# Optimization experiments

Measured on AMD Instinct MI355X. Metric: run time of the kernel, lower is better.

The kernel has to match this reference:

```python
import jax, jax.numpy as jnp
import numpy as np

F, V, D, B = 3, 512, 8192, 64


def setup_inputs() -> dict:
    key = jax.random.key(0)
    k1, k2 = jax.random.split(key)
    # bipolar (MAP) codebooks: (f, v, d) in {-1, +1}
    codebooks = jnp.sign(jax.random.normal(k1, (F, V, D), dtype=jnp.float32))
    codebooks = jnp.where(codebooks == 0, 1.0, codebooks)
    # ground-truth factors -> inputs = bind (elementwise product) of one codevector per factor
    idx = jax.random.randint(k2, (B, F), 0, V)
    picked = codebooks[jnp.arange(F)[None, :], idx]          # (b, f, d)
    inputs = jnp.prod(picked, axis=1)                         # (b, d)
    # init estimates: bundle (superposition) of each codebook, signed, broadcast to batch
    init = jnp.sign(jnp.sum(codebooks, axis=1))               # (f, d)
    init = jnp.where(init == 0, 1.0, init)
    init_estimates = jnp.broadcast_to(init, (B, F, D)).astype(jnp.float32)
    return {"inputs": inputs, "init_estimates": init_estimates,
            "codebooks": codebooks, "iterations": 10}


def reference(inputs, init_estimates, codebooks, iterations):
    f = init_estimates.shape[-2]

    def step(est):
        # MAP inverse is identity; inv_others[:, j] = prod_{i != j} est[:, i]
        rolled = jnp.stack([jnp.roll(est, i, axis=-2) for i in range(1, f)], axis=-2)  # (b,f,f-1,d)
        inv_others = jnp.prod(rolled, axis=-2)                 # (b, f, d)  multibind
        new_est = inputs[:, None, :] * inv_others              # bind       (b, f, d)
        sim = jnp.einsum('bfd,fvd->bfv', new_est, codebooks)   # codebook similarity
        return jnp.sign(jnp.einsum('bfv,fvd->bfd', sim, codebooks))

    def cond(c):
        est, old, cnt, done = c
        return (cnt < iterations) & jnp.logical_not(done)

    def body(c):
        est, old, cnt, done = c
        new = step(est)
        done = jnp.all(new == old)
        return (new, new, cnt + 1, done)

    carry0 = (init_estimates, init_estimates, jnp.int32(0), jnp.array(False))
    est, _, cnt, _ = jax.lax.while_loop(cond, body, carry0)

    # cleanup: nearest codevector per factor (argmax dot similarity)
    sims = jnp.einsum('bfd,fvd->bfv', est, codebooks)
    outcome = jnp.argmax(sims, axis=-1)                        # (b, f) int indices
    return outcome, cnt - 1
```

## Files before the change

kernel.cpp:

```cpp
#include <hip/hip_runtime.h>

#define F 3
#define V 512
#define D 8192
#define B 64
#define ITERS 10
#define DW 256

typedef __bf16 bf16_t;
typedef __bf16 bf16x8 __attribute__((ext_vector_type(8)));
typedef float f32x4 __attribute__((ext_vector_type(4)));
typedef unsigned int u32;
typedef unsigned long long u64;


__global__ __launch_bounds__(256) void k_init_tr(const float* __restrict__ Csrc,
                                                 bf16_t* __restrict__ CbT,
                                                 u32* __restrict__ Cbits) {
  int f = blockIdx.z, vt = blockIdx.y, dt = blockIdx.x;
  __shared__ bf16_t tile[64 * 65];
  int t = threadIdx.x;
  int lane = t & 63;
  int v0 = vt * 64, d0 = dt * 64;
#pragma unroll
  for (int p = 0; p < 16; ++p) {
    int q = t + 256 * p;
    int i = q >> 6, j = q & 63;
    float x = Csrc[((long)(f * V + v0 + i)) * D + d0 + j];
    tile[i * 65 + j] = (bf16_t)x;
    u64 bal = __ballot(x < 0.f);
    if (lane == 0) {
      int v = v0 + i;
      uint2 wp;
      wp.x = (u32)(bal & 0xffffffffull);
      wp.y = (u32)(bal >> 32);
      *(uint2*)&Cbits[(((f * 64 + (dt >> 1)) * 512) + v) * 4 + (dt & 1) * 2] = wp;
    }
  }
  __syncthreads();
#pragma unroll
  for (int p = 0; p < 16; ++p) {
    int q = t + 256 * p;
    int jj = q >> 6, ii = q & 63;
    CbT[((long)f * D + d0 + jj) * V + v0 + ii] = tile[ii * 65 + jj];
  }
}

__global__ void k_init_pack(const float* __restrict__ inputs, const float* __restrict__ ie,
                            u32* __restrict__ in_bits, u32* __restrict__ es0,
                            u32* __restrict__ ez0, int* __restrict__ flags) {
  int tid = blockIdx.x * blockDim.x + threadIdx.x;
  int lane = tid & 63;
  int gw = tid >> 6;
  int NW = (gridDim.x * blockDim.x) >> 6;
  const int IN_W = B * (D / 64);
  const int EST_W = B * F * (D / 64);
  for (int c = gw; c < IN_W + EST_W; c += NW) {
    if (c < IN_W) {
      int b = c >> 7, dc = c & 127;
      float x = inputs[(long)b * D + dc * 64 + lane];
      u64 bal = __ballot(x < 0.f);
      if (lane == 0) {
        in_bits[b * DW + dc * 2] = (u32)(bal & 0xffffffffull);
        in_bits[b * DW + dc * 2 + 1] = (u32)(bal >> 32);
      }
    } else {
      int cc = c - IN_W;
      int bf = cc >> 7, dc = cc & 127;
      float x = ie[(long)bf * D + dc * 64 + lane];
      u64 bs = __ballot(x < 0.f);
      u64 bz = __ballot(x == 0.f);
      if (lane == 0) {
        es0[bf * DW + dc * 2] = (u32)(bs & 0xffffffffull);
        es0[bf * DW + dc * 2 + 1] = (u32)(bs >> 32);
        ez0[bf * DW + dc * 2] = (u32)(bz & 0xffffffffull);
        ez0[bf * DW + dc * 2 + 1] = (u32)(bz >> 32);
      }
    }
  }
  if (tid < 32) flags[tid] = 0;
}

__global__ __launch_bounds__(256) void k_sim(const u32* __restrict__ Cbits,
                                             const u32* __restrict__ in_bits,
                                             const u32* __restrict__ es0,
                                             const u32* __restrict__ ez0,
                                             const u32* __restrict__ es1,
                                             const u32* __restrict__ ez1,
                                             int* __restrict__ simBase,
                                             const int* __restrict__ anydiff,
                                             const int* __restrict__ hzp, int iter) {
  const int t = threadIdx.x, lane = t & 63;
  const int gw = blockIdx.x * 4 + (t >> 6);
  const int vg = gw & 7, bp = (gw >> 3) & 31, f = gw >> 8;
  const int b0 = bp * 2;
  const bool is_final = (iter >= ITERS);
  const u32 *es, *ez;
  int* sim;
  if (is_final) {
    int first0 = ITERS;
    for (int i = 0; i < ITERS; ++i)
      if (anydiff[i] == 0) { first0 = i; break; }
    int par = (first0 < ITERS) ? ((first0 + 1) & 1) : 0;
    es = par ? es1 : es0;
    ez = par ? ez1 : ez0;
    sim = simBase + ITERS * (F * B * V);
  } else {
    for (int i = 0; i < iter; ++i)
      if (anydiff[i] == 0) return;
    es = (iter & 1) ? es1 : es0;
    ez = (iter & 1) ? ez1 : ez0;
    sim = simBase + iter * (F * B * V);
  }
  const int hz = *hzp;

  u32 As0[4], As1[4], Az0[4], Az1[4];
  if (is_final) {
    const int i0 = (b0 * F + f) * DW, i1 = ((b0 + 1) * F + f) * DW;
#pragma unroll
    for (int r = 0; r < 4; ++r) {
      int o = r * 64 + lane;
      As0[r] = es[i0 + o];
      As1[r] = es[i1 + o];
    }
    if (hz) {
#pragma unroll
      for (int r = 0; r < 4; ++r) {
        int o = r * 64 + lane;
        Az0[r] = ~ez[i0 + o];
        Az1[r] = ~ez[i1 + o];
      }
    }
  } else {
    const int f1 = (f + 1) % 3, f2 = (f + 2) % 3;
    const int a0 = (b0 * F + f1) * DW, a1 = (b0 * F + f2) * DW;
    const int c0 = ((b0 + 1) * F + f1) * DW, c1 = ((b0 + 1) * F + f2) * DW;
    const int n0 = b0 * DW, n1 = (b0 + 1) * DW;
#pragma unroll
    for (int r = 0; r < 4; ++r) {
      int o = r * 64 + lane;
      As0[r] = in_bits[n0 + o] ^ es[a0 + o] ^ es[a1 + o];
      As1[r] = in_bits[n1 + o] ^ es[c0 + o] ^ es[c1 + o];
    }
    if (hz) {
#pragma unroll
      for (int r = 0; r < 4; ++r) {
        int o = r * 64 + lane;
        Az0[r] = ~(ez[a0 + o] | ez[a1 + o]);
        Az1[r] = ~(ez[c0 + o] | ez[c1 + o]);
      }
    }
  }

  int nzc0 = D, nzc1 = D;
  if (hz) {
    int p0 = 0, p1 = 0;
#pragma unroll
    for (int r = 0; r < 4; ++r) {
      p0 += __popc(Az0[r]);
      p1 += __popc(Az1[r]);
    }
    for (int off = 32; off; off >>= 1) {
      p0 += __shfl_xor(p0, off, 64);
      p1 += __shfl_xor(p1, off, 64);
    }
    nzc0 = p0;
    nzc1 = p1;
  }

  int acc0 = 0, acc1 = 0;
  const uint4* Cp = (const uint4*)Cbits + ((long)f * 64) * 512 + vg * 64 + lane;
  if (!hz) {
#pragma unroll
    for (int r = 0; r < 4; ++r) {
#pragma unroll
      for (int i = 0; i < 16; ++i) {
        uint4 c = Cp[(r * 16 + i) * 512];
        const int k = i * 4;
        u32 a;
        a = (u32)__builtin_amdgcn_readlane((int)As0[r], k + 0); acc0 += __popc(c.x ^ a);
        a = (u32)__builtin_amdgcn_readlane((int)As0[r], k + 1); acc0 += __popc(c.y ^ a);
        a = (u32)__builtin_amdgcn_readlane((int)As0[r], k + 2); acc0 += __popc(c.z ^ a);
        a = (u32)__builtin_amdgcn_readlane((int)As0[r], k + 3); acc0 += __popc(c.w ^ a);
        a = (u32)__builtin_amdgcn_readlane((int)As1[r], k + 0); acc1 += __popc(c.x ^ a);
        a = (u32)__builtin_amdgcn_readlane((int)As1[r], k + 1); acc1 += __popc(c.y ^ a);
        a = (u32)__builtin_amdgcn_readlane((int)As1[r], k + 2); acc1 += __popc(c.z ^ a);
        a = (u32)__builtin_amdgcn_readlane((int)As1[r], k + 3); acc1 += __popc(c.w ^ a);
      }
    }
  } else {
#pragma unroll
    for (int r = 0; r < 4; ++r) {
#pragma unroll
      for (int i = 0; i < 16; ++i) {
        uint4 c = Cp[(r * 16 + i) * 512];
        const int k = i * 4;
        u32 a, z;
        a = (u32)__builtin_amdgcn_readlane((int)As0[r], k + 0);
        z = (u32)__builtin_amdgcn_readlane((int)Az0[r], k + 0); acc0 += __popc((c.x ^ a) & z);
        a = (u32)__builtin_amdgcn_readlane((int)As0[r], k + 1);
        z = (u32)__builtin_amdgcn_readlane((int)Az0[r], k + 1); acc0 += __popc((c.y ^ a) & z);
        a = (u32)__builtin_amdgcn_readlane((int)As0[r], k + 2);
        z = (u32)__builtin_amdgcn_readlane((int)Az0[r], k + 2); acc0 += __popc((c.z ^ a) & z);
        a = (u32)__builtin_amdgcn_readlane((int)As0[r], k + 3);
        z = (u32)__builtin_amdgcn_readlane((int)Az0[r], k + 3); acc0 += __popc((c.w ^ a) & z);
        a = (u32)__builtin_amdgcn_readlane((int)As1[r], k + 0);
        z = (u32)__builtin_amdgcn_readlane((int)Az1[r], k + 0); acc1 += __popc((c.x ^ a) & z);
        a = (u32)__builtin_amdgcn_readlane((int)As1[r], k + 1);
        z = (u32)__builtin_amdgcn_readlane((int)Az1[r], k + 1); acc1 += __popc((c.y ^ a) & z);
        a = (u32)__builtin_amdgcn_readlane((int)As1[r], k + 2);
        z = (u32)__builtin_amdgcn_readlane((int)Az1[r], k + 2); acc1 += __popc((c.z ^ a) & z);
        a = (u32)__builtin_amdgcn_readlane((int)As1[r], k + 3);
        z = (u32)__builtin_amdgcn_readlane((int)Az1[r], k + 3); acc1 += __popc((c.w ^ a) & z);
      }
    }
  }
  const int v = vg * 64 + lane;
  sim[(f * B + b0) * V + v] = nzc0 - 2 * acc0;
  sim[(f * B + b0 + 1) * V + v] = nzc1 - 2 * acc1;
}

__global__ __launch_bounds__(256) void k_upd(const int* __restrict__ simBase,
                                             const bf16_t* __restrict__ CbT,
                                             u32* __restrict__ es0, u32* __restrict__ ez0,
                                             u32* __restrict__ es1, u32* __restrict__ ez1,
                                             int* __restrict__ anydiff,
                                             int* __restrict__ hzp, int iter) {
  const int f = blockIdx.y;
  const int d0 = blockIdx.x * 128;
  for (int i = 0; i < iter; ++i)
    if (anydiff[i] == 0) return;
  const u32* esIn = (iter & 1) ? es1 : es0;
  const u32* ezIn = (iter & 1) ? ez1 : ez0;
  u32* esOut = (iter & 1) ? es0 : es1;
  u32* ezOut = (iter & 1) ? ez0 : ez1;
  const int* sim = simBase + iter * (F * B * V) + f * (B * V);

  __shared__ __attribute__((aligned(16))) bf16_t lAh[64 * 88];
  __shared__ __attribute__((aligned(16))) bf16_t lAl[64 * 88];
  __shared__ __attribute__((aligned(16))) bf16_t lB[128 * 88];

  const int t = threadIdx.x;
  const int lane = t & 63, w = t >> 6;
  const int lm = lane & 15, quad = lane >> 4;

  f32x4 zero = {0.f, 0.f, 0.f, 0.f};
  f32x4 accH[4][2], accL[4][2];
#pragma unroll
  for (int mt = 0; mt < 4; ++mt)
#pragma unroll
    for (int nt = 0; nt < 2; ++nt) { accH[mt][nt] = zero; accL[mt][nt] = zero; }

  for (int c = 0; c < 8; ++c) {
    const int vb = c * 64;
    __syncthreads();
#pragma unroll
    for (int p = 0; p < 2; ++p) {
      int q = t + 256 * p;
      int b = q >> 3, vv = (q & 7) * 8;
      const int* sp = sim + b * V + vb + vv;
#pragma unroll
      for (int i = 0; i < 8; ++i) {
        int si = sp[i];
        lAh[b * 88 + vv + i] = (bf16_t)(float)(si >> 8);
        lAl[b * 88 + vv + i] = (bf16_t)(float)(si & 255);
      }
    }
#pragma unroll
    for (int p = 0; p < 4; ++p) {
      int q = t + 256 * p;
      int r = q >> 3, vv = (q & 7) * 8;
      *(bf16x8*)&lB[r * 88 + vv] =
          *(const bf16x8*)(CbT + ((long)f * D + d0 + r) * V + vb + vv);
    }
    __syncthreads();
#pragma unroll
    for (int ks2 = 0; ks2 < 2; ++ks2) {
      const int kb = ks2 * 32 + quad * 8;
      bf16x8 bf0 = *(const bf16x8*)&lB[(w * 32 + lm) * 88 + kb];
      bf16x8 bf1 = *(const bf16x8*)&lB[(w * 32 + 16 + lm) * 88 + kb];
#pragma unroll
      for (int mt = 0; mt < 4; ++mt) {
        bf16x8 ah = *(const bf16x8*)&lAh[(mt * 16 + lm) * 88 + kb];
        bf16x8 al = *(const bf16x8*)&lAl[(mt * 16 + lm) * 88 + kb];
        accH[mt][0] = __builtin_amdgcn_mfma_f32_16x16x32_bf16(ah, bf0, accH[mt][0], 0, 0, 0);
        accH[mt][1] = __builtin_amdgcn_mfma_f32_16x16x32_bf16(ah, bf1, accH[mt][1], 0, 0, 0);
        accL[mt][0] = __builtin_amdgcn_mfma_f32_16x16x32_bf16(al, bf0, accL[mt][0], 0, 0, 0);
        accL[mt][1] = __builtin_amdgcn_mfma_f32_16x16x32_bf16(al, bf1, accL[mt][1], 0, 0, 0);
      }
    }
  }
  const int W = blockIdx.x * 4 + w;
  bool anyd = false, zf = false;
#pragma unroll
  for (int mt = 0; mt < 4; ++mt)
#pragma unroll
    for (int r = 0; r < 4; ++r) {
      float v0 = 256.f * accH[mt][0][r] + accL[mt][0][r];
      float v1 = 256.f * accH[mt][1][r] + accL[mt][1][r];
      u64 s0 = __ballot(v0 < 0.f);
      u64 s1 = __ballot(v1 < 0.f);
      u64 z0 = __ballot(v0 == 0.f);
      u64 z1 = __ballot(v1 == 0.f);
      zf |= ((z0 | z1) != 0ull);
      if (lm == 0) {
        u32 ws = (u32)((s0 >> (quad * 16)) & 0xffffull) |
                 (((u32)((s1 >> (quad * 16)) & 0xffffull)) << 16);
        u32 wz = (u32)((z0 >> (quad * 16)) & 0xffffull) |
                 (((u32)((z1 >> (quad * 16)) & 0xffffull)) << 16);
        int b = mt * 16 + quad * 4 + r;
        int idx = (b * F + f) * DW + W;
        esOut[idx] = ws;
        ezOut[idx] = wz;
        anyd |= (esIn[idx] != ws) || (ezIn[idx] != wz);
      }
    }
  if (__any(anyd) && lane == 0) atomicOr(&anydiff[iter], 1);
  if (zf && lane == 0) atomicOr(hzp, 1);
}

__global__ __launch_bounds__(64) void k_out(const int* __restrict__ simBase,
                                            const int* __restrict__ anydiff,
                                            int* __restrict__ out) {
  const int* sim = simBase + ITERS * (F * B * V);
  int bid = blockIdx.x;
  int b = bid / F, f = bid % F;
  int lane = threadIdx.x;
  const int* row = sim + (f * B + b) * V;
  int best = -2147483647;
  int bidx = 0;
#pragma unroll
  for (int i = 0; i < V / 64; ++i) {
    int v = lane + 64 * i;
    int x = row[v];
    if (x > best) { best = x; bidx = v; }
  }
  for (int off = 32; off; off >>= 1) {
    int ov = __shfl_down(best, off, 64);
    int oi = __shfl_down(bidx, off, 64);
    if (ov > best || (ov == best && oi < bidx)) { best = ov; bidx = oi; }
  }
  if (lane == 0) out[b * F + f] = bidx;
  if (bid == 0 && lane == 0) {
    int first0 = ITERS;
    for (int i = 0; i < ITERS; ++i) {
      if (anydiff[i] == 0) { first0 = i; break; }
    }
    int cnt = (first0 < ITERS) ? (first0 + 1) : ITERS;
    out[B * F] = cnt - 1;
  }
}

extern "C" void kernel_launch(void* const* d_in, const int* in_sizes, int n_in,
                              void* d_out, int out_size, void* d_ws, size_t ws_size,
                              hipStream_t stream) {
  const float* inputs    = (const float*)d_in[0];
  const float* init_est  = (const float*)d_in[1];
  const float* codebooks = (const float*)d_in[2];

  char* w = (char*)d_ws;
  size_t o = 0;
  auto alloc = [&](size_t bytes) -> void* {
    void* p = w + o;
    o = (o + bytes + 255) & ~(size_t)255;
    return p;
  };
  bf16_t* CbT  = (bf16_t*)alloc((size_t)F * D * V * 2);
  u32* Cbits   = (u32*)alloc((size_t)F * 64 * 512 * 4 * 4);
  u32* in_bits = (u32*)alloc((size_t)B * DW * 4);
  u32* es0     = (u32*)alloc((size_t)B * F * DW * 4);
  u32* ez0     = (u32*)alloc((size_t)B * F * DW * 4);
  u32* es1     = (u32*)alloc((size_t)B * F * DW * 4);
  u32* ez1     = (u32*)alloc((size_t)B * F * DW * 4);
  int* simBase = (int*)alloc((size_t)(ITERS + 1) * F * B * V * 4);
  int* flags   = (int*)alloc(128);
  int* anydiff = flags;
  int* hz      = flags + 16;

  k_init_tr<<<dim3(128, 8, 3), 256, 0, stream>>>(codebooks, CbT, Cbits);
  k_init_pack<<<1024, 256, 0, stream>>>(inputs, init_est, in_bits, es0, ez0, flags);

  for (int j = 0; j < ITERS; ++j) {
    k_sim<<<192, 256, 0, stream>>>(Cbits, in_bits, es0, ez0, es1, ez1, simBase, anydiff, hz, j);
    k_upd<<<dim3(64, 3), 256, 0, stream>>>(simBase, CbT, es0, ez0, es1, ez1, anydiff, hz, j);
  }
  k_sim<<<192, 256, 0, stream>>>(Cbits, in_bits, es0, ez0, es1, ez1, simBase, anydiff, hz, ITERS);
  k_out<<<B * F, 64, 0, stream>>>(simBase, anydiff, (int*)d_out);
}
```

Baseline: 498.6 us.

## Fuse iteration loop into one persistent kernel with software grid barriers

Replaces the 21 per-iteration sim/update launches plus the output kernel with one persistent kernel of 192 blocks. Blocks synchronise through an atomic counter/generation grid barrier, and the loop exits early on convergence instead of launching no-op kernels. This removes kernel launch gaps and shrinks the sim buffer to a single reused slot. Correctness now relies on all 192 blocks being co-resident, which a plain launch does not guarantee. Flag initialisation moves into k_init_tr, and the hz flag is now set from the initial estimates.

```diff
diff --git a/kernel.cpp b/kernel.cpp
--- a/kernel.cpp
+++ b/kernel.cpp
@@ -6,6 +6,7 @@
 #define B 64
 #define ITERS 10
 #define DW 256
+#define NBLK 192
 
 typedef __bf16 bf16_t;
 typedef __bf16 bf16x8 __attribute__((ext_vector_type(8)));
@@ -16,12 +17,14 @@
 
 __global__ __launch_bounds__(256) void k_init_tr(const float* __restrict__ Csrc,
                                                  bf16_t* __restrict__ CbT,
-                                                 u32* __restrict__ Cbits) {
+                                                 u32* __restrict__ Cbits,
+                                                 int* __restrict__ flags) {
   int f = blockIdx.z, vt = blockIdx.y, dt = blockIdx.x;
   __shared__ bf16_t tile[64 * 65];
   int t = threadIdx.x;
   int lane = t & 63;
   int v0 = vt * 64, d0 = dt * 64;
+  if (f == 0 && vt == 0 && dt == 0 && t < 32) flags[t] = 0;
 #pragma unroll
   for (int p = 0; p < 16; ++p) {
     int q = t + 256 * p;
@@ -75,278 +78,287 @@
         es0[bf * DW + dc * 2 + 1] = (u32)(bs >> 32);
         ez0[bf * DW + dc * 2] = (u32)(bz & 0xffffffffull);
         ez0[bf * DW + dc * 2 + 1] = (u32)(bz >> 32);
-      }
-    }
-  }
-  if (tid < 32) flags[tid] = 0;
-}
-
-__global__ __launch_bounds__(256) void k_sim(const u32* __restrict__ Cbits,
-                                             const u32* __restrict__ in_bits,
-                                             const u32* __restrict__ es0,
-                                             const u32* __restrict__ ez0,
-                                             const u32* __restrict__ es1,
-                                             const u32* __restrict__ ez1,
-                                             int* __restrict__ simBase,
-                                             const int* __restrict__ anydiff,
-                                             const int* __restrict__ hzp, int iter) {
-  const int t = threadIdx.x, lane = t & 63;
-  const int gw = blockIdx.x * 4 + (t >> 6);
-  const int vg = gw & 7, bp = (gw >> 3) & 31, f = gw >> 8;
-  const int b0 = bp * 2;
-  const bool is_final = (iter >= ITERS);
-  const u32 *es, *ez;
-  int* sim;
-  if (is_final) {
-    int first0 = ITERS;
-    for (int i = 0; i < ITERS; ++i)
-      if (anydiff[i] == 0) { first0 = i; break; }
-    int par = (first0 < ITERS) ? ((first0 + 1) & 1) : 0;
-    es = par ? es1 : es0;
-    ez = par ? ez1 : ez0;
-    sim = simBase + ITERS * (F * B * V);
-  } else {
-    for (int i = 0; i < iter; ++i)
-      if (anydiff[i] == 0) return;
-    es = (iter & 1) ? es1 : es0;
-    ez = (iter & 1) ? ez1 : ez0;
-    sim = simBase + iter * (F * B * V);
-  }
-  const int hz = *hzp;
-
-  u32 As0[4], As1[4], Az0[4], Az1[4];
-  if (is_final) {
-    const int i0 = (b0 * F + f) * DW, i1 = ((b0 + 1) * F + f) * DW;
-#pragma unroll
-    for (int r = 0; r < 4; ++r) {
-      int o = r * 64 + lane;
-      As0[r] = es[i0 + o];
-      As1[r] = es[i1 + o];
-    }
-    if (hz) {
-#pragma unroll
-      for (int r = 0; r < 4; ++r) {
-        int o = r * 64 + lane;
-        Az0[r] = ~ez[i0 + o];
-        Az1[r] = ~ez[i1 + o];
-      }
-    }
-  } else {
-    const int f1 = (f + 1) % 3, f2 = (f + 2) % 3;
-    const int a0 = (b0 * F + f1) * DW, a1 = (b0 * F + f2) * DW;
-    const int c0 = ((b0 + 1) * F + f1) * DW, c1 = ((b0 + 1) * F + f2) * DW;
-    const int n0 = b0 * DW, n1 = (b0 + 1) * DW;
-#pragma unroll
-    for (int r = 0; r < 4; ++r) {
-      int o = r * 64 + lane;
-      As0[r] = in_bits[n0 + o] ^ es[a0 + o] ^ es[a1 + o];
-      As1[r] = in_bits[n1 + o] ^ es[c0 + o] ^ es[c1 + o];
-    }
-    if (hz) {
-#pragma unroll
-      for (int r = 0; r < 4; ++r) {
-        int o = r * 64 + lane;
-        Az0[r] = ~(ez[a0 + o] | ez[a1 + o]);
-        Az1[r] = ~(ez[c0 + o] | ez[c1 + o]);
-      }
-    }
-  }
-
-  int nzc0 = D, nzc1 = D;
-  if (hz) {
-    int p0 = 0, p1 = 0;
-#pragma unroll
-    for (int r = 0; r < 4; ++r) {
-      p0 += __popc(Az0[r]);
-      p1 += __popc(Az1[r]);
-    }
-    for (int off = 32; off; off >>= 1) {
-      p0 += __shfl_xor(p0, off, 64);
-      p1 += __shfl_xor(p1, off, 64);
-    }
-    nzc0 = p0;
-    nzc1 = p1;
-  }
-
-  int acc0 = 0, acc1 = 0;
-  const uint4* Cp = (const uint4*)Cbits + ((long)f * 64) * 512 + vg * 64 + lane;
-  if (!hz) {
-#pragma unroll
-    for (int r = 0; r < 4; ++r) {
-#pragma unroll
-      for (int i = 0; i < 16; ++i) {
-        uint4 c = Cp[(r * 16 + i) * 512];
-        const int k = i * 4;
-        u32 a;
-        a = (u32)__builtin_amdgcn_readlane((int)As0[r], k + 0); acc0 += __popc(c.x ^ a);
-        a = (u32)__builtin_amdgcn_readlane((int)As0[r], k + 1); acc0 += __popc(c.y ^ a);
-        a = (u32)__builtin_amdgcn_readlane((int)As0[r], k + 2); acc0 += __popc(c.z ^ a);
-        a = (u32)__builtin_amdgcn_readlane((int)As0[r], k + 3); acc0 += __popc(c.w ^ a);
-        a = (u32)__builtin_amdgcn_readlane((int)As1[r], k + 0); acc1 += __popc(c.x ^ a);
-        a = (u32)__builtin_amdgcn_readlane((int)As1[r], k + 1); acc1 += __popc(c.y ^ a);
-        a = (u32)__builtin_amdgcn_readlane((int)As1[r], k + 2); acc1 += __popc(c.z ^ a);
-        a = (u32)__builtin_amdgcn_readlane((int)As1[r], k + 3); acc1 += __popc(c.w ^ a);
-      }
-    }
-  } else {
-#pragma unroll
-    for (int r = 0; r < 4; ++r) {
-#pragma unroll
-      for (int i = 0; i < 16; ++i) {
-        uint4 c = Cp[(r * 16 + i) * 512];
-        const int k = i * 4;
-        u32 a, z;
-        a = (u32)__builtin_amdgcn_readlane((int)As0[r], k + 0);
-        z = (u32)__builtin_amdgcn_readlane((int)Az0[r], k + 0); acc0 += __popc((c.x ^ a) & z);
-        a = (u32)__builtin_amdgcn_readlane((int)As0[r], k + 1);
-        z = (u32)__builtin_amdgcn_readlane((int)Az0[r], k + 1); acc0 += __popc((c.y ^ a) & z);
-        a = (u32)__builtin_amdgcn_readlane((int)As0[r], k + 2);
-        z = (u32)__builtin_amdgcn_readlane((int)Az0[r], k + 2); acc0 += __popc((c.z ^ a) & z);
-        a = (u32)__builtin_amdgcn_readlane((int)As0[r], k + 3);
-        z = (u32)__builtin_amdgcn_readlane((int)Az0[r], k + 3); acc0 += __popc((c.w ^ a) & z);
-        a = (u32)__builtin_amdgcn_readlane((int)As1[r], k + 0);
-        z = (u32)__builtin_amdgcn_readlane((int)Az1[r], k + 0); acc1 += __popc((c.x ^ a) & z);
-        a = (u32)__builtin_amdgcn_readlane((int)As1[r], k + 1);
-        z = (u32)__builtin_amdgcn_readlane((int)Az1[r], k + 1); acc1 += __popc((c.y ^ a) & z);
-        a = (u32)__builtin_amdgcn_readlane((int)As1[r], k + 2);
-        z = (u32)__builtin_amdgcn_readlane((int)Az1[r], k + 2); acc1 += __popc((c.z ^ a) & z);
-        a = (u32)__builtin_amdgcn_readlane((int)As1[r], k + 3);
-        z = (u32)__builtin_amdgcn_readlane((int)Az1[r], k + 3); acc1 += __popc((c.w ^ a) & z);
-      }
-    }
-  }
-  const int v = vg * 64 + lane;
-  sim[(f * B + b0) * V + v] = nzc0 - 2 * acc0;
-  sim[(f * B + b0 + 1) * V + v] = nzc1 - 2 * acc1;
-}
-
-__global__ __launch_bounds__(256) void k_upd(const int* __restrict__ simBase,
-                                             const bf16_t* __restrict__ CbT,
-                                             u32* __restrict__ es0, u32* __restrict__ ez0,
-                                             u32* __restrict__ es1, u32* __restrict__ ez1,
-                                             int* __restrict__ anydiff,
-                                             int* __restrict__ hzp, int iter) {
-  const int f = blockIdx.y;
-  const int d0 = blockIdx.x * 128;
-  for (int i = 0; i < iter; ++i)
-    if (anydiff[i] == 0) return;
-  const u32* esIn = (iter & 1) ? es1 : es0;
-  const u32* ezIn = (iter & 1) ? ez1 : ez0;
-  u32* esOut = (iter & 1) ? es0 : es1;
-  u32* ezOut = (iter & 1) ? ez0 : ez1;
-  const int* sim = simBase + iter * (F * B * V) + f * (B * V);
-
+        if (bz) atomicOr(&flags[16], 1);
+      }
+    }
+  }
+}
+
+__device__ inline void grid_sync(int* counter, int* gen) {
+  __syncthreads();
+  if (threadIdx.x == 0) {
+    __threadfence();
+    int g = __hip_atomic_load(gen, __ATOMIC_RELAXED, __HIP_MEMORY_SCOPE_AGENT);
+    int a = __hip_atomic_fetch_add(counter, 1, __ATOMIC_ACQ_REL, __HIP_MEMORY_SCOPE_AGENT);
+    if (a == NBLK - 1) {
+      __hip_atomic_store(counter, 0, __ATOMIC_RELAXED, __HIP_MEMORY_SCOPE_AGENT);
+      __hip_atomic_store(gen, g + 1, __ATOMIC_RELEASE, __HIP_MEMORY_SCOPE_AGENT);
+    } else {
+      while (__hip_atomic_load(gen, __ATOMIC_ACQUIRE, __HIP_MEMORY_SCOPE_AGENT) == g)
+        __builtin_amdgcn_s_sleep(2);
+    }
+    __threadfence();
+  }
+  __syncthreads();
+}
+
+__global__ __launch_bounds__(256) void k_fused(
+    const u32* __restrict__ Cbits, const u32* __restrict__ in_bits,
+    u32* __restrict__ es0, u32* __restrict__ ez0,
+    u32* __restrict__ es1, u32* __restrict__ ez1,
+    const bf16_t* __restrict__ CbT, int* __restrict__ sim,
+    int* __restrict__ flags, int* __restrict__ out) {
   __shared__ __attribute__((aligned(16))) bf16_t lAh[64 * 88];
   __shared__ __attribute__((aligned(16))) bf16_t lAl[64 * 88];
   __shared__ __attribute__((aligned(16))) bf16_t lB[128 * 88];
-
-  const int t = threadIdx.x;
-  const int lane = t & 63, w = t >> 6;
+  __shared__ int sh_hz, sh_conv;
+
+  int* bar_cnt = flags + 24;
+  int* bar_gen = flags + 25;
+
+  const int bid = blockIdx.x;
+  const int t = threadIdx.x, lane = t & 63, w = t >> 6;
   const int lm = lane & 15, quad = lane >> 4;
-
-  f32x4 zero = {0.f, 0.f, 0.f, 0.f};
-  f32x4 accH[4][2], accL[4][2];
-#pragma unroll
-  for (int mt = 0; mt < 4; ++mt)
-#pragma unroll
-    for (int nt = 0; nt < 2; ++nt) { accH[mt][nt] = zero; accL[mt][nt] = zero; }
-
-  for (int c = 0; c < 8; ++c) {
-    const int vb = c * 64;
+  const int gw = bid * 4 + w;
+  const int vg = gw & 7, bp = (gw >> 3) & 31, fs = gw >> 8;
+  const int b0 = bp * 2;
+  const int du = (bid & 63) * 128, fu = bid >> 6;
+
+  int parity = 0;
+  int done_iter = ITERS;
+
+  if (t == 0)
+    sh_hz = __hip_atomic_load(&flags[16], __ATOMIC_ACQUIRE, __HIP_MEMORY_SCOPE_AGENT);
+  __syncthreads();
+
+  auto sim_phase = [&](bool is_final, int hz) {
+    const u32* es = parity ? es1 : es0;
+    const u32* ez = parity ? ez1 : ez0;
+    u32 As0[4], As1[4], Az0[4], Az1[4];
+    if (is_final) {
+      const int i0 = (b0 * F + fs) * DW, i1 = ((b0 + 1) * F + fs) * DW;
+#pragma unroll
+      for (int r = 0; r < 4; ++r) {
+        int o = r * 64 + lane;
+        As0[r] = es[i0 + o];
+        As1[r] = es[i1 + o];
+      }
+      if (hz) {
+#pragma unroll
+        for (int r = 0; r < 4; ++r) {
+          int o = r * 64 + lane;
+          Az0[r] = ~ez[i0 + o];
+          Az1[r] = ~ez[i1 + o];
+        }
+      }
+    } else {
+      const int f1 = (fs + 1) % 3, f2 = (fs + 2) % 3;
+      const int a0 = (b0 * F + f1) * DW, a1 = (b0 * F + f2) * DW;
+      const int c0 = ((b0 + 1) * F + f1) * DW, c1 = ((b0 + 1) * F + f2) * DW;
+      const int n0 = b0 * DW, n1 = (b0 + 1) * DW;
+#pragma unroll
+      for (int r = 0; r < 4; ++r) {
+        int o = r * 64 + lane;
+        As0[r] = in_bits[n0 + o] ^ es[a0 + o] ^ es[a1 + o];
+        As1[r] = in_bits[n1 + o] ^ es[c0 + o] ^ es[c1 + o];
+      }
+      if (hz) {
+#pragma unroll
+        for (int r = 0; r < 4; ++r) {
+          int o = r * 64 + lane;
+          Az0[r] = ~(ez[a0 + o] | ez[a1 + o]);
+          Az1[r] = ~(ez[c0 + o] | ez[c1 + o]);
+        }
+      }
+    }
+
+    int nzc0 = D, nzc1 = D;
+    if (hz) {
+      int p0 = 0, p1 = 0;
+#pragma unroll
+      for (int r = 0; r < 4; ++r) {
+        p0 += __popc(Az0[r]);
+        p1 += __popc(Az1[r]);
+      }
+      for (int off = 32; off; off >>= 1) {
+        p0 += __shfl_xor(p0, off, 64);
+        p1 += __shfl_xor(p1, off, 64);
+      }
+      nzc0 = p0;
+      nzc1 = p1;
+    }
+
+    int acc0 = 0, acc1 = 0;
+    const uint4* Cp = (const uint4*)Cbits + ((long)fs * 64) * 512 + vg * 64 + lane;
+    if (!hz) {
+#pragma unroll
+      for (int r = 0; r < 4; ++r) {
+#pragma unroll
+        for (int i = 0; i < 16; ++i) {
+          uint4 c = Cp[(r * 16 + i) * 512];
+          const int k = i * 4;
+          u32 a;
+          a = (u32)__builtin_amdgcn_readlane((int)As0[r], k + 0); acc0 += __popc(c.x ^ a);
+          a = (u32)__builtin_amdgcn_readlane((int)As0[r], k + 1); acc0 += __popc(c.y ^ a);
+          a = (u32)__builtin_amdgcn_readlane((int)As0[r], k + 2); acc0 += __popc(c.z ^ a);
+          a = (u32)__builtin_amdgcn_readlane((int)As0[r], k + 3); acc0 += __popc(c.w ^ a);
+          a = (u32)__builtin_amdgcn_readlane((int)As1[r], k + 0); acc1 += __popc(c.x ^ a);
+          a = (u32)__builtin_amdgcn_readlane((int)As1[r], k + 1); acc1 += __popc(c.y ^ a);
+          a = (u32)__builtin_amdgcn_readlane((int)As1[r], k + 2); acc1 += __popc(c.z ^ a);
+          a = (u32)__builtin_amdgcn_readlane((int)As1[r], k + 3); acc1 += __popc(c.w ^ a);
+        }
+      }
+    } else {
+#pragma unroll
+      for (int r = 0; r < 4; ++r) {
+#pragma unroll
+        for (int i = 0; i < 16; ++i) {
+          uint4 c = Cp[(r * 16 + i) * 512];
+          const int k = i * 4;
+          u32 a, z;
+          a = (u32)__builtin_amdgcn_readlane((int)As0[r], k + 0);
+          z = (u32)__builtin_amdgcn_readlane((int)Az0[r], k + 0); acc0 += __popc((c.x ^ a) & z);
+          a = (u32)__builtin_amdgcn_readlane((int)As0[r], k + 1);
+          z = (u32)__builtin_amdgcn_readlane((int)Az0[r], k + 1); acc0 += __popc((c.y ^ a) & z);
+          a = (u32)__builtin_amdgcn_readlane((int)As0[r], k + 2);
+          z = (u32)__builtin_amdgcn_readlane((int)Az0[r], k + 2); acc0 += __popc((c.z ^ a) & z);
+          a = (u32)__builtin_amdgcn_readlane((int)As0[r], k + 3);
+          z = (u32)__builtin_amdgcn_readlane((int)Az0[r], k + 3); acc0 += __popc((c.w ^ a) & z);
+          a = (u32)__builtin_amdgcn_readlane((int)As1[r], k + 0);
+          z = (u32)__builtin_amdgcn_readlane((int)Az1[r], k + 0); acc1 += __popc((c.x ^ a) & z);
+          a = (u32)__builtin_amdgcn_readlane((int)As1[r], k + 1);
+          z = (u32)__builtin_amdgcn_readlane((int)Az1[r], k + 1); acc1 += __popc((c.y ^ a) & z);
+          a = (u32)__builtin_amdgcn_readlane((int)As1[r], k + 2);
+          z = (u32)__builtin_amdgcn_readlane((int)Az1[r], k + 2); acc1 += __popc((c.z ^ a) & z);
+          a = (u32)__builtin_amdgcn_readlane((int)As1[r], k + 3);
+          z = (u32)__builtin_amdgcn_readlane((int)Az1[r], k + 3); acc1 += __popc((c.w ^ a) & z);
+        }
+      }
+    }
+    const int v = vg * 64 + lane;
+    sim[(fs * B + b0) * V + v] = nzc0 - 2 * acc0;
+    sim[(fs * B + b0 + 1) * V + v] = nzc1 - 2 * acc1;
+  };
+
+  auto upd_phase = [&](int j) {
+    const u32* esIn = parity ? es1 : es0;
+    const u32* ezIn = parity ? ez1 : ez0;
+    u32* esOut = parity ? es0 : es1;
+    u32* ezOut = parity ? ez0 : ez1;
+    const int* simf = sim + fu * (B * V);
+
+    f32x4 zero = {0.f, 0.f, 0.f, 0.f};
+    f32x4 accH[4][2], accL[4][2];
+#pragma unroll
+    for (int mt = 0; mt < 4; ++mt)
+#pragma unroll
+      for (int nt = 0; nt < 2; ++nt) { accH[mt][nt] = zero; accL[mt][nt] = zero; }
+
+    for (int c = 0; c < 8; ++c) {
+      const int vb = c * 64;
+      __syncthreads();
+#pragma unroll
+      for (int p = 0; p < 2; ++p) {
+        int q = t + 256 * p;
+        int b = q >> 3, vv = (q & 7) * 8;
+        const int* sp = simf + b * V + vb + vv;
+#pragma unroll
+        for (int i = 0; i < 8; ++i) {
+          int si = sp[i];
+          lAh[b * 88 + vv + i] = (bf16_t)(float)(si >> 8);
+          lAl[b * 88 + vv + i] = (bf16_t)(float)(si & 255);
+        }
+      }
+#pragma unroll
+      for (int p = 0; p < 4; ++p) {
+        int q = t + 256 * p;
+        int r = q >> 3, vv = (q & 7) * 8;
+        *(bf16x8*)&lB[r * 88 + vv] =
+            *(const bf16x8*)(CbT + ((long)fu * D + du + r) * V + vb + vv);
+      }
+      __syncthreads();
+#pragma unroll
+      for (int ks2 = 0; ks2 < 2; ++ks2) {
+        const int kb = ks2 * 32 + quad * 8;
+        bf16x8 bf0 = *(const bf16x8*)&lB[(w * 32 + lm) * 88 + kb];
+        bf16x8 bf1 = *(const bf16x8*)&lB[(w * 32 + 16 + lm) * 88 + kb];
+#pragma unroll
+        for (int mt = 0; mt < 4; ++mt) {
+          bf16x8 ah = *(const bf16x8*)&lAh[(mt * 16 + lm) * 88 + kb];
+          bf16x8 al = *(const bf16x8*)&lAl[(mt * 16 + lm) * 88 + kb];
+          accH[mt][0] = __builtin_amdgcn_mfma_f32_16x16x32_bf16(ah, bf0, accH[mt][0], 0, 0, 0);
+          accH[mt][1] = __builtin_amdgcn_mfma_f32_16x16x32_bf16(ah, bf1, accH[mt][1], 0, 0, 0);
+          accL[mt][0] = __builtin_amdgcn_mfma_f32_16x16x32_bf16(al, bf0, accL[mt][0], 0, 0, 0);
+          accL[mt][1] = __builtin_amdgcn_mfma_f32_16x16x32_bf16(al, bf1, accL[mt][1], 0, 0, 0);
+        }
+      }
+    }
+    const int W = (bid & 63) * 4 + w;
+    bool anyd = false, zf = false;
+#pragma unroll
+    for (int mt = 0; mt < 4; ++mt)
+#pragma unroll
+      for (int r = 0; r < 4; ++r) {
+        float v0 = 256.f * accH[mt][0][r] + accL[mt][0][r];
+        float v1 = 256.f * accH[mt][1][r] + accL[mt][1][r];
+        u64 s0 = __ballot(v0 < 0.f);
+        u64 s1 = __ballot(v1 < 0.f);
+        u64 z0 = __ballot(v0 == 0.f);
+        u64 z1 = __ballot(v1 == 0.f);
+        zf |= ((z0 | z1) != 0ull);
+        if (lm == 0) {
+          u32 ws = (u32)((s0 >> (quad * 16)) & 0xffffull) |
+                   (((u32)((s1 >> (quad * 16)) & 0xffffull)) << 16);
+          u32 wz = (u32)((z0 >> (quad * 16)) & 0xffffull) |
+                   (((u32)((z1 >> (quad * 16)) & 0xffffull)) << 16);
+          int b = mt * 16 + quad * 4 + r;
+          int idx = (b * F + fu) * DW + W;
+          esOut[idx] = ws;
+          ezOut[idx] = wz;
+          anyd |= (esIn[idx] != ws) || (ezIn[idx] != wz);
+        }
+      }
+    if (__any(anyd) && lane == 0) atomicOr(&flags[j], 1);
+    if (zf && lane == 0) atomicOr(&flags[16], 1);
+  };
+
+  for (int j = 0; j < ITERS; ++j) {
+    sim_phase(false, sh_hz);
+    grid_sync(bar_cnt, bar_gen);
+    upd_phase(j);
+    grid_sync(bar_cnt, bar_gen);
+    if (t == 0) {
+      sh_conv = __hip_atomic_load(&flags[j], __ATOMIC_ACQUIRE, __HIP_MEMORY_SCOPE_AGENT);
+      sh_hz = __hip_atomic_load(&flags[16], __ATOMIC_ACQUIRE, __HIP_MEMORY_SCOPE_AGENT);
+    }
     __syncthreads();
-#pragma unroll
-    for (int p = 0; p < 2; ++p) {
-      int q = t + 256 * p;
-      int b = q >> 3, vv = (q & 7) * 8;
-      const int* sp = sim + b * V + vb + vv;
-#pragma unroll
-      for (int i = 0; i < 8; ++i) {
-        int si = sp[i];
-        lAh[b * 88 + vv + i] = (bf16_t)(float)(si >> 8);
-        lAl[b * 88 + vv + i] = (bf16_t)(float)(si & 255);
-      }
-    }
-#pragma unroll
-    for (int p = 0; p < 4; ++p) {
-      int q = t + 256 * p;
-      int r = q >> 3, vv = (q & 7) * 8;
-      *(bf16x8*)&lB[r * 88 + vv] =
-          *(const bf16x8*)(CbT + ((long)f * D + d0 + r) * V + vb + vv);
-    }
-    __syncthreads();
-#pragma unroll
-    for (int ks2 = 0; ks2 < 2; ++ks2) {
-      const int kb = ks2 * 32 + quad * 8;
-      bf16x8 bf0 = *(const bf16x8*)&lB[(w * 32 + lm) * 88 + kb];
-      bf16x8 bf1 = *(const bf16x8*)&lB[(w * 32 + 16 + lm) * 88 + kb];
-#pragma unroll
-      for (int mt = 0; mt < 4; ++mt) {
-        bf16x8 ah = *(const bf16x8*)&lAh[(mt * 16 + lm) * 88 + kb];
-        bf16x8 al = *(const bf16x8*)&lAl[(mt * 16 + lm) * 88 + kb];
-        accH[mt][0] = __builtin_amdgcn_mfma_f32_16x16x32_bf16(ah, bf0, accH[mt][0], 0, 0, 0);
-        accH[mt][1] = __builtin_amdgcn_mfma_f32_16x16x32_bf16(ah, bf1, accH[mt][1], 0, 0, 0);
-        accL[mt][0] = __builtin_amdgcn_mfma_f32_16x16x32_bf16(al, bf0, accL[mt][0], 0, 0, 0);
-        accL[mt][1] = __builtin_amdgcn_mfma_f32_16x16x32_bf16(al, bf1, accL[mt][1], 0, 0, 0);
-      }
-    }
-  }
-  const int W = blockIdx.x * 4 + w;
-  bool anyd = false, zf = false;
-#pragma unroll
-  for (int mt = 0; mt < 4; ++mt)
-#pragma unroll
-    for (int r = 0; r < 4; ++r) {
-      float v0 = 256.f * accH[mt][0][r] + accL[mt][0][r];
-      float v1 = 256.f * accH[mt][1][r] + accL[mt][1][r];
-      u64 s0 = __ballot(v0 < 0.f);
-      u64 s1 = __ballot(v1 < 0.f);
-      u64 z0 = __ballot(v0 == 0.f);
-      u64 z1 = __ballot(v1 == 0.f);
-      zf |= ((z0 | z1) != 0ull);
-      if (lm == 0) {
-        u32 ws = (u32)((s0 >> (quad * 16)) & 0xffffull) |
-                 (((u32)((s1 >> (quad * 16)) & 0xffffull)) << 16);
-        u32 wz = (u32)((z0 >> (quad * 16)) & 0xffffull) |
-                 (((u32)((z1 >> (quad * 16)) & 0xffffull)) << 16);
-        int b = mt * 16 + quad * 4 + r;
-        int idx = (b * F + f) * DW + W;
-        esOut[idx] = ws;
-        ezOut[idx] = wz;
-        anyd |= (esIn[idx] != ws) || (ezIn[idx] != wz);
-      }
-    }
-  if (__any(anyd) && lane == 0) atomicOr(&anydiff[iter], 1);
-  if (zf && lane == 0) atomicOr(hzp, 1);
-}
-
-__global__ __launch_bounds__(64) void k_out(const int* __restrict__ simBase,
-                                            const int* __restrict__ anydiff,
-                                            int* __restrict__ out) {
-  const int* sim = simBase + ITERS * (F * B * V);
-  int bid = blockIdx.x;
-  int b = bid / F, f = bid % F;
-  int lane = threadIdx.x;
-  const int* row = sim + (f * B + b) * V;
-  int best = -2147483647;
-  int bidx = 0;
-#pragma unroll
-  for (int i = 0; i < V / 64; ++i) {
-    int v = lane + 64 * i;
-    int x = row[v];
-    if (x > best) { best = x; bidx = v; }
-  }
-  for (int off = 32; off; off >>= 1) {
-    int ov = __shfl_down(best, off, 64);
-    int oi = __shfl_down(bidx, off, 64);
-    if (ov > best || (ov == best && oi < bidx)) { best = ov; bidx = oi; }
-  }
-  if (lane == 0) out[b * F + f] = bidx;
-  if (bid == 0 && lane == 0) {
-    int first0 = ITERS;
-    for (int i = 0; i < ITERS; ++i) {
-      if (anydiff[i] == 0) { first0 = i; break; }
-    }
-    int cnt = (first0 < ITERS) ? (first0 + 1) : ITERS;
+    parity ^= 1;
+    if (sh_conv == 0) { done_iter = j; break; }
+  }
+
+  sim_phase(true, sh_hz);
+  grid_sync(bar_cnt, bar_gen);
+
+  if (t < 64) {
+    int b = bid / F, f = bid % F;
+    const int* row = sim + (f * B + b) * V;
+    int best = -2147483647;
+    int bidx = 0;
+#pragma unroll
+    for (int i = 0; i < V / 64; ++i) {
+      int v = lane + 64 * i;
+      int x = row[v];
+      if (x > best) { best = x; bidx = v; }
+    }
+    for (int off = 32; off; off >>= 1) {
+      int ov = __shfl_down(best, off, 64);
+      int oi = __shfl_down(bidx, off, 64);
+      if (ov > best || (ov == best && oi < bidx)) { best = ov; bidx = oi; }
+    }
+    if (lane == 0) out[b * F + f] = bidx;
+  }
+  if (bid == 0 && t == 0) {
+    int cnt = (done_iter < ITERS) ? (done_iter + 1) : ITERS;
     out[B * F] = cnt - 1;
   }
 }
@@ -372,18 +384,11 @@
   u32* ez0     = (u32*)alloc((size_t)B * F * DW * 4);
   u32* es1     = (u32*)alloc((size_t)B * F * DW * 4);
   u32* ez1     = (u32*)alloc((size_t)B * F * DW * 4);
-  int* simBase = (int*)alloc((size_t)(ITERS + 1) * F * B * V * 4);
+  int* sim     = (int*)alloc((size_t)F * B * V * 4);
   int* flags   = (int*)alloc(128);
-  int* anydiff = flags;
-  int* hz      = flags + 16;
-
-  k_init_tr<<<dim3(128, 8, 3), 256, 0, stream>>>(codebooks, CbT, Cbits);
+
+  k_init_tr<<<dim3(128, 8, 3), 256, 0, stream>>>(codebooks, CbT, Cbits, flags);
   k_init_pack<<<1024, 256, 0, stream>>>(inputs, init_est, in_bits, es0, ez0, flags);
-
-  for (int j = 0; j < ITERS; ++j) {
-    k_sim<<<192, 256, 0, stream>>>(Cbits, in_bits, es0, ez0, es1, ez1, simBase, anydiff, hz, j);
-    k_upd<<<dim3(64, 3), 256, 0, stream>>>(simBase, CbT, es0, ez0, es1, ez1, anydiff, hz, j);
-  }
-  k_sim<<<192, 256, 0, stream>>>(Cbits, in_bits, es0, ez0, es1, ez1, simBase, anydiff, hz, ITERS);
-  k_out<<<B * F, 64, 0, stream>>>(simBase, anydiff, (int*)d_out);
-}
+  k_fused<<<NBLK, 256, 0, stream>>>(Cbits, in_bits, es0, ez0, es1, ez1, CbT, sim,
+                                    flags, (int*)d_out);
+}
```

After: 1.223 ms. 145% more time.
